# Optimization experiments

Measured on AMD Instinct MI355X. Metric: run time of the kernel, lower is better.

## Reference

```python
import jax, jax.numpy as jnp
import numpy as np

NUM_INTERVALS = 101
HW_EMBED_DIM = 10
NUM_DEVICES = 50


def setup_inputs() -> dict:
    key = jax.random.key(0)
    k1, k2, k3, k4 = jax.random.split(key, 4)
    x = jax.random.uniform(k1, (1, 1), dtype=jnp.float32)            # scalar control in [0,1]
    hw = jax.random.normal(k2, (HW_EMBED_DIM,), dtype=jnp.float32)   # hardware query vector
    hw_emb = jax.random.normal(k3, (NUM_DEVICES, HW_EMBED_DIM), dtype=jnp.float32)      # hardware_embedding.weight
    expert_emb = jax.random.normal(k4, (NUM_DEVICES, NUM_INTERVALS, 30), dtype=jnp.float32)  # stacked per-expert embedding tables
    return {"x": x, "hw": hw, "hw_emb": hw_emb, "expert_emb": expert_emb}


def reference(x, hw, hw_emb, expert_emb):
    # similarity = squeeze(hw @ W^T) / sqrt(d); sin-softmax gate over 50 experts
    sim = jnp.matmul(hw, hw_emb.T) / jnp.sqrt(jnp.float32(HW_EMBED_DIM))  # [50]
    gate = jax.nn.softmax(jnp.sin(sim), axis=-1)                          # [50]

    # Every expert looks up the SAME data-dependent row index derived from x[0,0].
    idx = jnp.round(x[0, 0] * (NUM_INTERVALS - 1)).astype(jnp.int32)      # scalar index in [0,100]
    rows = expert_emb[:, idx, :]                                          # [50, 30] batched gather (fused, no loop)

    # softmax-weighted accumulation of the 50 expert outputs
    out = jnp.einsum('e,ed->d', gate, rows).reshape(6, 5)
    return out
```

## Files before the change

kernel.cpp:

```cpp
#include <hip/hip_runtime.h>
#include <math.h>

#define NUM_DEVICES   50
#define HW_DIM        10
#define NUM_INTERVALS 101
#define ROW_DIM       30

__global__ __launch_bounds__(64)
void mhn_kernel(const float* __restrict__ x,
                const float* __restrict__ hw,
                const float* __restrict__ hw_emb,
                const float* __restrict__ expert_emb,
                float* __restrict__ out)
{
    __shared__ float gate_s[NUM_DEVICES];
    const int lane = threadIdx.x;

    float s = -INFINITY;
    if (lane < NUM_DEVICES) {
        float acc = 0.f;
#pragma unroll
        for (int j = 0; j < HW_DIM; ++j)
            acc = fmaf(hw[j], hw_emb[lane * HW_DIM + j], acc);
        s = sinf(acc * 0.31622776601683794f);
    }

    float m = s;
#pragma unroll
    for (int off = 32; off >= 1; off >>= 1)
        m = fmaxf(m, __shfl_xor(m, off, 64));

    float e = (lane < NUM_DEVICES) ? expf(s - m) : 0.f;
    float sum = e;
#pragma unroll
    for (int off = 32; off >= 1; off >>= 1)
        sum += __shfl_xor(sum, off, 64);

    if (lane < NUM_DEVICES) gate_s[lane] = e / sum;
    __syncthreads();

    const int idx = (int)rintf(x[0] * (float)(NUM_INTERVALS - 1));
    if (lane < ROW_DIM) {
        const float* rows = expert_emb + (size_t)idx * ROW_DIM + lane;
        float acc = 0.f;
#pragma unroll 10
        for (int ee = 0; ee < NUM_DEVICES; ++ee)
            acc = fmaf(gate_s[ee], rows[(size_t)ee * (NUM_INTERVALS * ROW_DIM)], acc);
        out[lane] = acc;
    }
}

extern "C" void kernel_launch(void* const* d_in, const int* in_sizes, int n_in,
                              void* d_out, int out_size, void* d_ws, size_t ws_size,
                              hipStream_t stream)
{
    const float* x          = (const float*)d_in[0];
    const float* hw         = (const float*)d_in[1];
    const float* hw_emb     = (const float*)d_in[2];
    const float* expert_emb = (const float*)d_in[3];
    float* out              = (float*)d_out;

    mhn_kernel<<<1, 64, 0, stream>>>(x, hw, hw_emb, expert_emb, out);
}
```

Before: 62.74 us.

## Prefetch all expert rows before gate softmax and broadcast gates via shuffles

Issues all 50 expert-row loads into registers at kernel start, alongside the hw and hw_emb loads, so their memory latency overlaps the similarity, sine and softmax computation instead of following it serially. Shared memory and __syncthreads are replaced by wavefront __shfl broadcasts of the unnormalized gate values, and the division by the softmax sum is applied once at the end. This raises register pressure (50 floats per lane) and has every lane load rows, with lanes past the row width clamped to a duplicate address.

```diff
diff --git a/kernel.cpp b/kernel.cpp
--- a/kernel.cpp
+++ b/kernel.cpp
@@ -5,6 +5,7 @@
 #define HW_DIM        10
 #define NUM_INTERVALS 101
 #define ROW_DIM       30
+#define EXPERT_STRIDE (NUM_INTERVALS * ROW_DIM)
 
 __global__ __launch_bounds__(64)
 void mhn_kernel(const float* __restrict__ x,
@@ -13,41 +14,53 @@
                 const float* __restrict__ expert_emb,
                 float* __restrict__ out)
 {
-    __shared__ float gate_s[NUM_DEVICES];
     const int lane = threadIdx.x;
 
-    float s = -INFINITY;
-    if (lane < NUM_DEVICES) {
-        float acc = 0.f;
+    const float xv = x[0];
+
+    float hw_r[HW_DIM];
+    float he_r[HW_DIM];
+    const float* he = hw_emb + (lane < NUM_DEVICES ? lane : 0) * HW_DIM;
 #pragma unroll
-        for (int j = 0; j < HW_DIM; ++j)
-            acc = fmaf(hw[j], hw_emb[lane * HW_DIM + j], acc);
-        s = sinf(acc * 0.31622776601683794f);
-    }
+    for (int j = 0; j < HW_DIM; ++j) hw_r[j] = hw[j];
+#pragma unroll
+    for (int j = 0; j < HW_DIM; ++j) he_r[j] = he[j];
+
+    const int idx = (int)rintf(xv * (float)(NUM_INTERVALS - 1));
+    const int d = (lane < ROW_DIM) ? lane : 0;
+    const float* rowp = expert_emb + (size_t)idx * ROW_DIM + d;
+    float r[NUM_DEVICES];
+#pragma unroll
+    for (int e = 0; e < NUM_DEVICES; ++e)
+        r[e] = rowp[(size_t)e * EXPERT_STRIDE];
+
+    float acc = 0.f;
+#pragma unroll
+    for (int j = 0; j < HW_DIM; ++j)
+        acc = fmaf(hw_r[j], he_r[j], acc);
+    const float s = (lane < NUM_DEVICES)
+                        ? sinf(acc * 0.31622776601683794f)
+                        : -INFINITY;
 
     float m = s;
 #pragma unroll
     for (int off = 32; off >= 1; off >>= 1)
         m = fmaxf(m, __shfl_xor(m, off, 64));
 
-    float e = (lane < NUM_DEVICES) ? expf(s - m) : 0.f;
-    float sum = e;
+    const float ev = (lane < NUM_DEVICES) ? expf(s - m) : 0.f;
+    float sum = ev;
 #pragma unroll
     for (int off = 32; off >= 1; off >>= 1)
         sum += __shfl_xor(sum, off, 64);
 
-    if (lane < NUM_DEVICES) gate_s[lane] = e / sum;
-    __syncthreads();
-
-    const int idx = (int)rintf(x[0] * (float)(NUM_INTERVALS - 1));
-    if (lane < ROW_DIM) {
-        const float* rows = expert_emb + (size_t)idx * ROW_DIM + lane;
-        float acc = 0.f;
-#pragma unroll 10
-        for (int ee = 0; ee < NUM_DEVICES; ++ee)
-            acc = fmaf(gate_s[ee], rows[(size_t)ee * (NUM_INTERVALS * ROW_DIM)], acc);
-        out[lane] = acc;
+    float o = 0.f;
+#pragma unroll
+    for (int e = 0; e < NUM_DEVICES; ++e) {
+        const float g = __shfl(ev, e, 64);
+        o = fmaf(g, r[e], o);
     }
+    if (lane < ROW_DIM)
+        out[lane] = o / sum;
 }
 
 extern "C" void kernel_launch(void* const* d_in, const int* in_sizes, int n_in,
```

Result: no change. 61.79 us (-1.5%).
